# Kernel optimization log

Measured on AMD Instinct MI355X. Metric: run time of the kernel, lower is better.

Reference implementation:

```python
import jax, jax.numpy as jnp
import numpy as np

VV = 100000   # value vocab
VP = 100000   # path vocab
VT = 50257    # tag vocab
E = 128       # embedding size
B = 2048      # batch of functions
N = 10        # rep_size (contexts per function)


def setup_inputs() -> dict:
    key = jax.random.key(0)
    ks = jax.random.split(key, 10)
    return {
        "value1_idx": jax.random.randint(ks[0], (B, N), 0, VV),
        "path_idx": jax.random.randint(ks[1], (B, N), 0, VP),
        "value2_idx": jax.random.randint(ks[2], (B, N), 0, VV),
        "value_emb": jax.random.normal(ks[3], (VV, E), jnp.float32) * 0.02,
        "path_emb": jax.random.normal(ks[4], (VP, E), jnp.float32) * 0.02,
        "tag_emb": jax.random.normal(ks[5], (VT, E), jnp.float32) * 0.02,
        "W_fc": jax.random.normal(ks[6], (3 * E, E), jnp.float32) * 0.02,
        "b_fc": jnp.zeros((E,), jnp.float32),
        "w_att": jax.random.normal(ks[7], (E,), jnp.float32) * 0.02,
        "b_att": jnp.zeros((), jnp.float32),
    }


def reference(value1_idx, path_idx, value2_idx, value_emb, path_emb, tag_emb,
              W_fc, b_fc, w_att, b_att):
    # Per-context embedding gathers: [B, N, E]
    v1 = value_emb[value1_idx]
    p = path_emb[path_idx]
    v2 = value_emb[value2_idx]
    ctx = jnp.concatenate([v1, p, v2], axis=-1)          # [B, N, 3E]
    c_tilde = jnp.tanh(ctx @ W_fc + b_fc)                # [B, N, E]
    # Attention pooling over the N contexts
    att = jax.nn.softmax(c_tilde @ w_att + b_att, axis=1)  # [B, N]
    v = jnp.einsum('bne,bn->be', c_tilde, att)           # [B, E]
    # Softmax classifier over all tags
    logits = v @ tag_emb.T                               # [B, VT]
    q = jax.nn.softmax(logits, axis=-1)
    return q
```

## Files before the change

### kernel.cpp

```cpp
#include <hip/hip_runtime.h>
#include <hip/hip_bf16.h>
#include <math.h>

#define VTAG 50257
#define EDIM 128
#define NREP 10
#define BFUNC 2048
#define NSTRIP 786
#define NPAD (NSTRIP * 64)

typedef __bf16 bf16x8 __attribute__((ext_vector_type(8)));
typedef float f32x4 __attribute__((ext_vector_type(4)));

__device__ __forceinline__ unsigned short f2bf(float x) {
    unsigned u = __float_as_uint(x);
    unsigned r = (u + 0x7fffu + ((u >> 16) & 1u)) >> 16;
    return (unsigned short)r;
}

__global__ __launch_bounds__(128) void k1_attn(
    const int* __restrict__ v1i, const int* __restrict__ pti,
    const int* __restrict__ v2i,
    const float* __restrict__ vemb, const float* __restrict__ pemb,
    const float* __restrict__ Wfc, const float* __restrict__ bfc,
    const float* __restrict__ watt, const float* __restrict__ batt,
    unsigned short* __restrict__ vbf)
{
    const int b = blockIdx.x;
    const int e = threadIdx.x;
    __shared__ float ctx[NREP][3 * EDIM];
    __shared__ float red[2][NREP];

    #pragma unroll
    for (int j = 0; j < 30; ++j) {
        int i = j * 128 + e;
        int n = i / 384;
        int c = i - n * 384;
        float val;
        if (c < 128)      val = vemb[(size_t)v1i[b * NREP + n] * EDIM + c];
        else if (c < 256) val = pemb[(size_t)pti[b * NREP + n] * EDIM + (c - 128)];
        else              val = vemb[(size_t)v2i[b * NREP + n] * EDIM + (c - 256)];
        ctx[n][c] = val;
    }
    __syncthreads();

    float acc[NREP];
    #pragma unroll
    for (int n = 0; n < NREP; ++n) acc[n] = 0.f;

    for (int k = 0; k < 384; k += 4) {
        float w0 = Wfc[(k + 0) * EDIM + e];
        float w1 = Wfc[(k + 1) * EDIM + e];
        float w2 = Wfc[(k + 2) * EDIM + e];
        float w3 = Wfc[(k + 3) * EDIM + e];
        #pragma unroll
        for (int n = 0; n < NREP; ++n) {
            float4 c4 = *(const float4*)&ctx[n][k];
            acc[n] = fmaf(c4.x, w0, acc[n]);
            acc[n] = fmaf(c4.y, w1, acc[n]);
            acc[n] = fmaf(c4.z, w2, acc[n]);
            acc[n] = fmaf(c4.w, w3, acc[n]);
        }
    }

    const float bias = bfc[e];
    const float we = watt[e];
    float ct[NREP];
    #pragma unroll
    for (int n = 0; n < NREP; ++n) ct[n] = tanhf(acc[n] + bias);

    const int wv = e >> 6, ln = e & 63;
    #pragma unroll
    for (int n = 0; n < NREP; ++n) {
        float p = ct[n] * we;
        p += __shfl_xor(p, 32);
        p += __shfl_xor(p, 16);
        p += __shfl_xor(p, 8);
        p += __shfl_xor(p, 4);
        p += __shfl_xor(p, 2);
        p += __shfl_xor(p, 1);
        if (ln == 0) red[wv][n] = p;
    }
    __syncthreads();

    const float batt0 = batt[0];
    float al[NREP];
    float m = -1e30f;
    #pragma unroll
    for (int n = 0; n < NREP; ++n) {
        al[n] = red[0][n] + red[1][n] + batt0;
        m = fmaxf(m, al[n]);
    }
    float s = 0.f;
    #pragma unroll
    for (int n = 0; n < NREP; ++n) { al[n] = __expf(al[n] - m); s += al[n]; }
    const float inv = 1.f / s;

    float v = 0.f;
    #pragma unroll
    for (int n = 0; n < NREP; ++n) v = fmaf(al[n] * inv, ct[n], v);

    vbf[b * EDIM + e] = f2bf(v);
}

__global__ __launch_bounds__(256) void k_conv_tag(
    const float* __restrict__ tag, unsigned short* __restrict__ tbf)
{
    size_t i = ((size_t)blockIdx.x * 256 + threadIdx.x) * 4;
    if (i >= (size_t)NPAD * EDIM) return;
    float4 x = make_float4(0.f, 0.f, 0.f, 0.f);
    if (i < (size_t)VTAG * EDIM) x = *(const float4*)(tag + i);
    ushort4 o;
    o.x = f2bf(x.x); o.y = f2bf(x.y); o.z = f2bf(x.z); o.w = f2bf(x.w);
    *(ushort4*)(tbf + i) = o;
}

__global__ __launch_bounds__(256) void k2_logits(
    const unsigned short* __restrict__ vbf, const unsigned short* __restrict__ tbf,
    float* __restrict__ out, float* __restrict__ pmax, float* __restrict__ psum)
{
    const int wave = threadIdx.x >> 6;
    const int lane = threadIdx.x & 63;
    const int quad = lane >> 4;
    const int l16  = lane & 15;
    const int strip = blockIdx.y;
    const int n0 = strip * 64;
    const int rowbase = blockIdx.x * 128 + wave * 32;

    const bf16x8* tb8 = (const bf16x8*)tbf;
    const bf16x8* vb8 = (const bf16x8*)vbf;

    bf16x8 bfrag[4][4];
    #pragma unroll
    for (int nt = 0; nt < 4; ++nt) {
        int col = n0 + nt * 16 + l16;
        const bf16x8* p = tb8 + (size_t)col * 16 + quad;
        #pragma unroll
        for (int ks = 0; ks < 4; ++ks) bfrag[nt][ks] = p[ks * 4];
    }
    bf16x8 afrag[2][4];
    #pragma unroll
    for (int mt = 0; mt < 2; ++mt) {
        int row = rowbase + mt * 16 + l16;
        const bf16x8* p = vb8 + (size_t)row * 16 + quad;
        #pragma unroll
        for (int ks = 0; ks < 4; ++ks) afrag[mt][ks] = p[ks * 4];
    }

    f32x4 acc[2][4];
    #pragma unroll
    for (int mt = 0; mt < 2; ++mt)
        #pragma unroll
        for (int nt = 0; nt < 4; ++nt) acc[mt][nt] = (f32x4){0.f, 0.f, 0.f, 0.f};

    #pragma unroll
    for (int ks = 0; ks < 4; ++ks)
        #pragma unroll
        for (int mt = 0; mt < 2; ++mt)
            #pragma unroll
            for (int nt = 0; nt < 4; ++nt)
                acc[mt][nt] = __builtin_amdgcn_mfma_f32_16x16x32_bf16(
                    afrag[mt][ks], bfrag[nt][ks], acc[mt][nt], 0, 0, 0);

    #pragma unroll
    for (int mt = 0; mt < 2; ++mt) {
        #pragma unroll
        for (int r = 0; r < 4; ++r) {
            const int row = rowbase + mt * 16 + quad * 4 + r;
            float lm = -1e30f;
            #pragma unroll
            for (int nt = 0; nt < 4; ++nt) {
                int col = n0 + nt * 16 + l16;
                float x = acc[mt][nt][r];
                if (col < VTAG) lm = fmaxf(lm, x);
            }
            lm = fmaxf(lm, __shfl_xor(lm, 1));
            lm = fmaxf(lm, __shfl_xor(lm, 2));
            lm = fmaxf(lm, __shfl_xor(lm, 4));
            lm = fmaxf(lm, __shfl_xor(lm, 8));
            float ls = 0.f;
            #pragma unroll
            for (int nt = 0; nt < 4; ++nt) {
                int col = n0 + nt * 16 + l16;
                float x = acc[mt][nt][r];
                if (col < VTAG) {
                    ls += __expf(x - lm);
                    out[(size_t)row * VTAG + col] = x;
                }
            }
            ls += __shfl_xor(ls, 1);
            ls += __shfl_xor(ls, 2);
            ls += __shfl_xor(ls, 4);
            ls += __shfl_xor(ls, 8);
            if (l16 == 0) {
                pmax[(size_t)row * NSTRIP + strip] = lm;
                psum[(size_t)row * NSTRIP + strip] = ls;
            }
        }
    }
}

__global__ __launch_bounds__(256) void k3_reduce(
    const float* __restrict__ pmax, const float* __restrict__ psum,
    float* __restrict__ rowM, float* __restrict__ rowR)
{
    const int row = blockIdx.x * 4 + (threadIdx.x >> 6);
    const int ln = threadIdx.x & 63;
    const float* pm = pmax + (size_t)row * NSTRIP;
    const float* ps = psum + (size_t)row * NSTRIP;

    float m = -1e30f;
    for (int i = ln; i < NSTRIP; i += 64) m = fmaxf(m, pm[i]);
    m = fmaxf(m, __shfl_xor(m, 32));
    m = fmaxf(m, __shfl_xor(m, 16));
    m = fmaxf(m, __shfl_xor(m, 8));
    m = fmaxf(m, __shfl_xor(m, 4));
    m = fmaxf(m, __shfl_xor(m, 2));
    m = fmaxf(m, __shfl_xor(m, 1));

    float s = 0.f;
    for (int i = ln; i < NSTRIP; i += 64) s += ps[i] * __expf(pm[i] - m);
    s += __shfl_xor(s, 32);
    s += __shfl_xor(s, 16);
    s += __shfl_xor(s, 8);
    s += __shfl_xor(s, 4);
    s += __shfl_xor(s, 2);
    s += __shfl_xor(s, 1);

    if (ln == 0) { rowM[row] = m; rowR[row] = 1.f / s; }
}

__global__ __launch_bounds__(256) void k4_norm(
    float* __restrict__ out, const float* __restrict__ rowM,
    const float* __restrict__ rowR)
{
    unsigned i0 = (blockIdx.x * 256u + threadIdx.x) * 4u;
    const unsigned total = (unsigned)BFUNC * VTAG;
    if (i0 >= total) return;
    unsigned row = i0 / VTAG;
    unsigned c = i0 - row * VTAG;
    if (c + 4 <= VTAG) {
        float M = rowM[row], R = rowR[row];
        float4 x = *(float4*)(out + i0);
        x.x = __expf(x.x - M) * R;
        x.y = __expf(x.y - M) * R;
        x.z = __expf(x.z - M) * R;
        x.w = __expf(x.w - M) * R;
        *(float4*)(out + i0) = x;
    } else {
        #pragma unroll
        for (int j = 0; j < 4; ++j) {
            unsigned i = i0 + j;
            unsigned r2 = i / VTAG;
            out[i] = __expf(out[i] - rowM[r2]) * rowR[r2];
        }
    }
}

extern "C" void kernel_launch(void* const* d_in, const int* in_sizes, int n_in,
                              void* d_out, int out_size, void* d_ws, size_t ws_size,
                              hipStream_t stream)
{
    const int*   v1i  = (const int*)d_in[0];
    const int*   pti  = (const int*)d_in[1];
    const int*   v2i  = (const int*)d_in[2];
    const float* vemb = (const float*)d_in[3];
    const float* pemb = (const float*)d_in[4];
    const float* temb = (const float*)d_in[5];
    const float* Wfc  = (const float*)d_in[6];
    const float* bfc  = (const float*)d_in[7];
    const float* watt = (const float*)d_in[8];
    const float* batt = (const float*)d_in[9];
    float* out = (float*)d_out;

    char* ws = (char*)d_ws;
    const size_t vbf_off  = 0;
    const size_t tbf_off  = vbf_off + 524288;
    const size_t pmax_off = tbf_off + 12877824;
    const size_t psum_off = pmax_off + 6438912;
    const size_t rowm_off = psum_off + 6438912;
    const size_t rowr_off = rowm_off + 8192;

    unsigned short* vbf = (unsigned short*)(ws + vbf_off);
    unsigned short* tbf = (unsigned short*)(ws + tbf_off);
    float* pmax = (float*)(ws + pmax_off);
    float* psum = (float*)(ws + psum_off);
    float* rowM = (float*)(ws + rowm_off);
    float* rowR = (float*)(ws + rowr_off);

    hipLaunchKernelGGL(k1_attn, dim3(BFUNC), dim3(128), 0, stream,
                       v1i, pti, v2i, vemb, pemb, Wfc, bfc, watt, batt, vbf);
    hipLaunchKernelGGL(k_conv_tag, dim3((NPAD * EDIM / 4 + 255) / 256), dim3(256),
                       0, stream, temb, tbf);
    hipLaunchKernelGGL(k2_logits, dim3(BFUNC / 128, NSTRIP), dim3(256), 0, stream,
                       vbf, tbf, out, pmax, psum);
    hipLaunchKernelGGL(k3_reduce, dim3(BFUNC / 4), dim3(256), 0, stream,
                       pmax, psum, rowM, rowR);
    hipLaunchKernelGGL(k4_norm, dim3(((unsigned)BFUNC * VTAG / 4 + 255) / 256),
                       dim3(256), 0, stream, out, rowM, rowR);
}
```

Measured before the change: 817.7 us.

## Recompute logits in a second pass instead of storing and re-reading them

The logits kernel is split into two passes. The first computes only per-strip max and sum partials. The second recomputes the bf16 MFMA logits and writes the normalized softmax directly, so the separate normalization kernel and the round-trip of the full 2048x50257 fp32 logits through memory go away. The attention kernel is also restructured so each wave handles one function with float4 gathers and no cross-wave reduction sync. The cost is running the GEMM twice, which is cheap at K=128.

```diff
diff --git a/kernel.cpp b/kernel.cpp
--- a/kernel.cpp
+++ b/kernel.cpp
@@ -26,81 +26,92 @@
     const float* __restrict__ watt, const float* __restrict__ batt,
     unsigned short* __restrict__ vbf)
 {
-    const int b = blockIdx.x;
-    const int e = threadIdx.x;
-    __shared__ float ctx[NREP][3 * EDIM];
-    __shared__ float red[2][NREP];
-
-    #pragma unroll
-    for (int j = 0; j < 30; ++j) {
-        int i = j * 128 + e;
-        int n = i / 384;
-        int c = i - n * 384;
-        float val;
-        if (c < 128)      val = vemb[(size_t)v1i[b * NREP + n] * EDIM + c];
-        else if (c < 256) val = pemb[(size_t)pti[b * NREP + n] * EDIM + (c - 128)];
-        else              val = vemb[(size_t)v2i[b * NREP + n] * EDIM + (c - 256)];
-        ctx[n][c] = val;
+    const int w  = threadIdx.x >> 6;
+    const int ln = threadIdx.x & 63;
+    const int b  = blockIdx.x * 2 + w;
+    __shared__ float ctx[2][NREP][3 * EDIM];
+
+    const int base = b * NREP;
+    #pragma unroll
+    for (int j = 0; j < 15; ++j) {
+        int i4 = j * 64 + ln;
+        int n  = i4 / 96;
+        int c4 = i4 - n * 96;
+        int c  = c4 * 4;
+        const float* src;
+        if (c4 < 32)      src = vemb + (size_t)v1i[base + n] * EDIM + c;
+        else if (c4 < 64) src = pemb + (size_t)pti[base + n] * EDIM + (c - 128);
+        else              src = vemb + (size_t)v2i[base + n] * EDIM + (c - 256);
+        *(float4*)&ctx[w][n][c] = *(const float4*)src;
     }
     __syncthreads();
 
-    float acc[NREP];
-    #pragma unroll
-    for (int n = 0; n < NREP; ++n) acc[n] = 0.f;
+    float acc0[NREP], acc1[NREP];
+    #pragma unroll
+    for (int n = 0; n < NREP; ++n) { acc0[n] = 0.f; acc1[n] = 0.f; }
 
     for (int k = 0; k < 384; k += 4) {
-        float w0 = Wfc[(k + 0) * EDIM + e];
-        float w1 = Wfc[(k + 1) * EDIM + e];
-        float w2 = Wfc[(k + 2) * EDIM + e];
-        float w3 = Wfc[(k + 3) * EDIM + e];
+        float wa0 = Wfc[(k + 0) * EDIM + ln];
+        float wa1 = Wfc[(k + 1) * EDIM + ln];
+        float wa2 = Wfc[(k + 2) * EDIM + ln];
+        float wa3 = Wfc[(k + 3) * EDIM + ln];
+        float wb0 = Wfc[(k + 0) * EDIM + ln + 64];
+        float wb1 = Wfc[(k + 1) * EDIM + ln + 64];
+        float wb2 = Wfc[(k + 2) * EDIM + ln + 64];
+        float wb3 = Wfc[(k + 3) * EDIM + ln + 64];
         #pragma unroll
         for (int n = 0; n < NREP; ++n) {
-            float4 c4 = *(const float4*)&ctx[n][k];
-            acc[n] = fmaf(c4.x, w0, acc[n]);
-            acc[n] = fmaf(c4.y, w1, acc[n]);
-            acc[n] = fmaf(c4.z, w2, acc[n]);
-            acc[n] = fmaf(c4.w, w3, acc[n]);
+            float4 c4 = *(const float4*)&ctx[w][n][k];
+            acc0[n] = fmaf(c4.x, wa0, acc0[n]);
+            acc0[n] = fmaf(c4.y, wa1, acc0[n]);
+            acc0[n] = fmaf(c4.z, wa2, acc0[n]);
+            acc0[n] = fmaf(c4.w, wa3, acc0[n]);
+            acc1[n] = fmaf(c4.x, wb0, acc1[n]);
+            acc1[n] = fmaf(c4.y, wb1, acc1[n]);
+            acc1[n] = fmaf(c4.z, wb2, acc1[n]);
+            acc1[n] = fmaf(c4.w, wb3, acc1[n]);
         }
     }
 
-    const float bias = bfc[e];
-    const float we = watt[e];
-    float ct[NREP];
-    #pragma unroll
-    for (int n = 0; n < NREP; ++n) ct[n] = tanhf(acc[n] + bias);
-
-    const int wv = e >> 6, ln = e & 63;
+    const float b0 = bfc[ln],       b1 = bfc[ln + 64];
+    const float wat0 = watt[ln],    wat1 = watt[ln + 64];
+    const float batt0 = batt[0];
+
+    float ct0[NREP], ct1[NREP];
     #pragma unroll
     for (int n = 0; n < NREP; ++n) {
-        float p = ct[n] * we;
+        ct0[n] = tanhf(acc0[n] + b0);
+        ct1[n] = tanhf(acc1[n] + b1);
+    }
+
+    float a[NREP];
+    float m = -1e30f;
+    #pragma unroll
+    for (int n = 0; n < NREP; ++n) {
+        float p = ct0[n] * wat0 + ct1[n] * wat1;
         p += __shfl_xor(p, 32);
         p += __shfl_xor(p, 16);
         p += __shfl_xor(p, 8);
         p += __shfl_xor(p, 4);
         p += __shfl_xor(p, 2);
         p += __shfl_xor(p, 1);
-        if (ln == 0) red[wv][n] = p;
-    }
-    __syncthreads();
-
-    const float batt0 = batt[0];
-    float al[NREP];
-    float m = -1e30f;
+        a[n] = p + batt0;
+        m = fmaxf(m, a[n]);
+    }
+    float s = 0.f;
+    #pragma unroll
+    for (int n = 0; n < NREP; ++n) { a[n] = __expf(a[n] - m); s += a[n]; }
+    const float inv = 1.f / s;
+
+    float v0 = 0.f, v1 = 0.f;
     #pragma unroll
     for (int n = 0; n < NREP; ++n) {
-        al[n] = red[0][n] + red[1][n] + batt0;
-        m = fmaxf(m, al[n]);
-    }
-    float s = 0.f;
-    #pragma unroll
-    for (int n = 0; n < NREP; ++n) { al[n] = __expf(al[n] - m); s += al[n]; }
-    const float inv = 1.f / s;
-
-    float v = 0.f;
-    #pragma unroll
-    for (int n = 0; n < NREP; ++n) v = fmaf(al[n] * inv, ct[n], v);
-
-    vbf[b * EDIM + e] = f2bf(v);
+        float at = a[n] * inv;
+        v0 = fmaf(at, ct0[n], v0);
+        v1 = fmaf(at, ct1[n], v1);
+    }
+    vbf[b * EDIM + ln]      = f2bf(v0);
+    vbf[b * EDIM + ln + 64] = f2bf(v1);
 }
 
 __global__ __launch_bounds__(256) void k_conv_tag(
@@ -115,9 +126,48 @@
     *(ushort4*)(tbf + i) = o;
 }
 
-__global__ __launch_bounds__(256) void k2_logits(
+__device__ __forceinline__ void mfma_logits(
     const unsigned short* __restrict__ vbf, const unsigned short* __restrict__ tbf,
-    float* __restrict__ out, float* __restrict__ pmax, float* __restrict__ psum)
+    int rowbase, int n0, int quad, int l16, f32x4 acc[2][4])
+{
+    const bf16x8* tb8 = (const bf16x8*)tbf;
+    const bf16x8* vb8 = (const bf16x8*)vbf;
+
+    bf16x8 bfrag[4][4];
+    #pragma unroll
+    for (int nt = 0; nt < 4; ++nt) {
+        int col = n0 + nt * 16 + l16;
+        const bf16x8* p = tb8 + (size_t)col * 16 + quad;
+        #pragma unroll
+        for (int ks = 0; ks < 4; ++ks) bfrag[nt][ks] = p[ks * 4];
+    }
+    bf16x8 afrag[2][4];
+    #pragma unroll
+    for (int mt = 0; mt < 2; ++mt) {
+        int row = rowbase + mt * 16 + l16;
+        const bf16x8* p = vb8 + (size_t)row * 16 + quad;
+        #pragma unroll
+        for (int ks = 0; ks < 4; ++ks) afrag[mt][ks] = p[ks * 4];
+    }
+
+    #pragma unroll
+    for (int mt = 0; mt < 2; ++mt)
+        #pragma unroll
+        for (int nt = 0; nt < 4; ++nt) acc[mt][nt] = (f32x4){0.f, 0.f, 0.f, 0.f};
+
+    #pragma unroll
+    for (int ks = 0; ks < 4; ++ks)
+        #pragma unroll
+        for (int mt = 0; mt < 2; ++mt)
+            #pragma unroll
+            for (int nt = 0; nt < 4; ++nt)
+                acc[mt][nt] = __builtin_amdgcn_mfma_f32_16x16x32_bf16(
+                    afrag[mt][ks], bfrag[nt][ks], acc[mt][nt], 0, 0, 0);
+}
+
+__global__ __launch_bounds__(256) void k2a_partials(
+    const unsigned short* __restrict__ vbf, const unsigned short* __restrict__ tbf,
+    float* __restrict__ pmax, float* __restrict__ psum)
 {
     const int wave = threadIdx.x >> 6;
     const int lane = threadIdx.x & 63;
@@ -127,40 +177,8 @@
     const int n0 = strip * 64;
     const int rowbase = blockIdx.x * 128 + wave * 32;
 
-    const bf16x8* tb8 = (const bf16x8*)tbf;
-    const bf16x8* vb8 = (const bf16x8*)vbf;
-
-    bf16x8 bfrag[4][4];
-    #pragma unroll
-    for (int nt = 0; nt < 4; ++nt) {
-        int col = n0 + nt * 16 + l16;
-        const bf16x8* p = tb8 + (size_t)col * 16 + quad;
-        #pragma unroll
-        for (int ks = 0; ks < 4; ++ks) bfrag[nt][ks] = p[ks * 4];
-    }
-    bf16x8 afrag[2][4];
-    #pragma unroll
-    for (int mt = 0; mt < 2; ++mt) {
-        int row = rowbase + mt * 16 + l16;
-        const bf16x8* p = vb8 + (size_t)row * 16 + quad;
-        #pragma unroll
-        for (int ks = 0; ks < 4; ++ks) afrag[mt][ks] = p[ks * 4];
-    }
-
     f32x4 acc[2][4];
-    #pragma unroll
-    for (int mt = 0; mt < 2; ++mt)
-        #pragma unroll
-        for (int nt = 0; nt < 4; ++nt) acc[mt][nt] = (f32x4){0.f, 0.f, 0.f, 0.f};
-
-    #pragma unroll
-    for (int ks = 0; ks < 4; ++ks)
-        #pragma unroll
-        for (int mt = 0; mt < 2; ++mt)
-            #pragma unroll
-            for (int nt = 0; nt < 4; ++nt)
-                acc[mt][nt] = __builtin_amdgcn_mfma_f32_16x16x32_bf16(
-                    afrag[mt][ks], bfrag[nt][ks], acc[mt][nt], 0, 0, 0);
+    mfma_logits(vbf, tbf, rowbase, n0, quad, l16, acc);
 
     #pragma unroll
     for (int mt = 0; mt < 2; ++mt) {
@@ -171,8 +189,7 @@
             #pragma unroll
             for (int nt = 0; nt < 4; ++nt) {
                 int col = n0 + nt * 16 + l16;
-                float x = acc[mt][nt][r];
-                if (col < VTAG) lm = fmaxf(lm, x);
+                if (col < VTAG) lm = fmaxf(lm, acc[mt][nt][r]);
             }
             lm = fmaxf(lm, __shfl_xor(lm, 1));
             lm = fmaxf(lm, __shfl_xor(lm, 2));
@@ -182,11 +199,7 @@
             #pragma unroll
             for (int nt = 0; nt < 4; ++nt) {
                 int col = n0 + nt * 16 + l16;
-                float x = acc[mt][nt][r];
-                if (col < VTAG) {
-                    ls += __expf(x - lm);
-                    out[(size_t)row * VTAG + col] = x;
-                }
+                if (col < VTAG) ls += __expf(acc[mt][nt][r] - lm);
             }
             ls += __shfl_xor(ls, 1);
             ls += __shfl_xor(ls, 2);
@@ -230,29 +243,35 @@
     if (ln == 0) { rowM[row] = m; rowR[row] = 1.f / s; }
 }
 
-__global__ __launch_bounds__(256) void k4_norm(
-    float* __restrict__ out, const float* __restrict__ rowM,
-    const float* __restrict__ rowR)
-{
-    unsigned i0 = (blockIdx.x * 256u + threadIdx.x) * 4u;
-    const unsigned total = (unsigned)BFUNC * VTAG;
-    if (i0 >= total) return;
-    unsigned row = i0 / VTAG;
-    unsigned c = i0 - row * VTAG;
-    if (c + 4 <= VTAG) {
-        float M = rowM[row], R = rowR[row];
-        float4 x = *(float4*)(out + i0);
-        x.x = __expf(x.x - M) * R;
-        x.y = __expf(x.y - M) * R;
-        x.z = __expf(x.z - M) * R;
-        x.w = __expf(x.w - M) * R;
-        *(float4*)(out + i0) = x;
-    } else {
-        #pragma unroll
-        for (int j = 0; j < 4; ++j) {
-            unsigned i = i0 + j;
-            unsigned r2 = i / VTAG;
-            out[i] = __expf(out[i] - rowM[r2]) * rowR[r2];
+__global__ __launch_bounds__(256) void k2b_write(
+    const unsigned short* __restrict__ vbf, const unsigned short* __restrict__ tbf,
+    const float* __restrict__ rowM, const float* __restrict__ rowR,
+    float* __restrict__ out)
+{
+    const int wave = threadIdx.x >> 6;
+    const int lane = threadIdx.x & 63;
+    const int quad = lane >> 4;
+    const int l16  = lane & 15;
+    const int strip = blockIdx.y;
+    const int n0 = strip * 64;
+    const int rowbase = blockIdx.x * 128 + wave * 32;
+
+    f32x4 acc[2][4];
+    mfma_logits(vbf, tbf, rowbase, n0, quad, l16, acc);
+
+    #pragma unroll
+    for (int mt = 0; mt < 2; ++mt) {
+        #pragma unroll
+        for (int r = 0; r < 4; ++r) {
+            const int row = rowbase + mt * 16 + quad * 4 + r;
+            const float M = rowM[row];
+            const float R = rowR[row];
+            #pragma unroll
+            for (int nt = 0; nt < 4; ++nt) {
+                int col = n0 + nt * 16 + l16;
+                if (col < VTAG)
+                    out[(size_t)row * VTAG + col] = __expf(acc[mt][nt][r] - M) * R;
+            }
         }
     }
 }
@@ -288,14 +307,14 @@
     float* rowM = (float*)(ws + rowm_off);
     float* rowR = (float*)(ws + rowr_off);
 
-    hipLaunchKernelGGL(k1_attn, dim3(BFUNC), dim3(128), 0, stream,
+    hipLaunchKernelGGL(k1_attn, dim3(BFUNC / 2), dim3(128), 0, stream,
                        v1i, pti, v2i, vemb, pemb, Wfc, bfc, watt, batt, vbf);
     hipLaunchKernelGGL(k_conv_tag, dim3((NPAD * EDIM / 4 + 255) / 256), dim3(256),
                        0, stream, temb, tbf);
-    hipLaunchKernelGGL(k2_logits, dim3(BFUNC / 128, NSTRIP), dim3(256), 0, stream,
-                       vbf, tbf, out, pmax, psum);
+    hipLaunchKernelGGL(k2a_partials, dim3(BFUNC / 128, NSTRIP), dim3(256), 0, stream,
+                       vbf, tbf, pmax, psum);
     hipLaunchKernelGGL(k3_reduce, dim3(BFUNC / 4), dim3(256), 0, stream,
                        pmax, psum, rowM, rowR);
-    hipLaunchKernelGGL(k4_norm, dim3(((unsigned)BFUNC * VTAG / 4 + 255) / 256),
-                       dim3(256), 0, stream, out, rowM, rowR);
-}
+    hipLaunchKernelGGL(k2b_write, dim3(BFUNC / 128, NSTRIP), dim3(256), 0, stream,
+                       vbf, tbf, rowM, rowR, out);
+}
```

New measurement: 844.0 us. +3.2%, slower.
